# Kernel tuning notes

Measured on AMD Instinct MI355X. Metric: run time of the kernel, lower is better.

Reference implementation:

```python
import jax, jax.numpy as jnp
import numpy as np

NUM_EXPERTS = 8
TOP_K = 2


def setup_inputs() -> dict:
    key = jax.random.key(0)
    ks = jax.random.split(key, 5)
    B, S, H, F, E = 2, 2048, 1024, 4096, NUM_EXPERTS
    return {
        "hidden_states": jax.random.normal(ks[0], (B, S, H), dtype=jnp.float32),
        "router_w": jax.random.normal(ks[1], (H, E), dtype=jnp.float32) * 0.02,
        "router_b": jnp.zeros((E,), dtype=jnp.float32),
        "w1": jax.random.normal(ks[2], (E, H, F), dtype=jnp.float32) * 0.02,
        "b1": jnp.zeros((E, F), dtype=jnp.float32),
        "w2": jax.random.normal(ks[3], (E, F, H), dtype=jnp.float32) * 0.02,
        "b2": jnp.zeros((E, H), dtype=jnp.float32),
    }


def reference(hidden_states, router_w, router_b, w1, b1, w2, b2):
    # Router: softmax over experts, take top-2, renormalize.
    logits = jnp.einsum("bsh,he->bse", hidden_states, router_w) + router_b
    probs = jax.nn.softmax(logits, axis=-1)
    top_w, top_i = jax.lax.top_k(probs, TOP_K)              # [B,S,2]
    top_w = top_w / jnp.sum(top_w, axis=-1, keepdims=True)
    # Combine weights per expert: [B,S,E] (sum of slot weights where routed).
    combine = jnp.sum(
        top_w[..., None] * jax.nn.one_hot(top_i, NUM_EXPERTS, dtype=top_w.dtype),
        axis=-2,
    )
    # Dense expert FFN over stacked experts (grouped GEMM form).
    h = jax.nn.gelu(
        jnp.einsum("bsh,ehf->ebsf", hidden_states, w1) + b1[:, None, None, :],
        approximate=False,
    )  # exact GELU matches torch nn.GELU default
    y = jnp.einsum("ebsf,efh->ebsh", h, w2) + b2[:, None, None, :]
    # Weighted combine of top-2 expert outputs per token.
    return jnp.einsum("bse,ebsh->bsh", combine, y)
```

## Files before the change

kernel.cpp:

```cpp
#include <hip/hip_runtime.h>
#include <hip/hip_bf16.h>
#include <stdint.h>

#define T_TOKENS 4096
#define H_DIM    1024
#define F_DIM    4096
#define NE       8
#define NA       8192

typedef __bf16 bf16x8 __attribute__((ext_vector_type(8)));
typedef float  f32x4  __attribute__((ext_vector_type(4)));

__device__ __forceinline__ float b2f(unsigned short u) {
    union { float f; uint32_t i; } v; v.i = ((uint32_t)u) << 16; return v.f;
}
__device__ __forceinline__ unsigned short f2b(float f) {
    union { float f; uint32_t i; } v; v.f = f;
    uint32_t x = v.i;
    return (unsigned short)((x + 0x7FFFu + ((x >> 16) & 1u)) >> 16);
}

__device__ __forceinline__ float gelu_f(float x) {
    float z = fabsf(x) * 0.70710678118f;
    float t = 1.0f / (1.0f + 0.3275911f * z);
    float p = t * (0.254829592f + t * (-0.284496736f +
              t * (1.421413741f + t * (-1.453152027f + t * 1.061405429f))));
    float erf_z = 1.0f - p * __expf(-z * z);
    float sgn_erf = (x >= 0.f) ? erf_z : -erf_z;
    return x * (0.5f + 0.5f * sgn_erf);
}

__device__ __forceinline__ void gl_lds16(const void* g, void* l) {
    __builtin_amdgcn_global_load_lds(
        (const __attribute__((address_space(1))) void*)g,
        (__attribute__((address_space(3))) void*)l,
        16, 0, 0);
}

__global__ void probe_kernel(const unsigned short* __restrict__ hs,
                             int* __restrict__ flag) {
    int lane = threadIdx.x;
    int cnt = 0;
    for (int j = 0; j < 16; j++) {
        unsigned short u = hs[(lane * 16 + j) * 2];
        int e = (u >> 7) & 0xFF;
        if (e >= 100 && e <= 135) cnt++;
    }
    for (int off = 32; off > 0; off >>= 1) cnt += __shfl_down(cnt, off);
    if (lane == 0) *flag = (cnt >= 512) ? 0 : 1;
}

__global__ __launch_bounds__(256) void router_kernel(
    const void* __restrict__ hs, const void* __restrict__ rw,
    const void* __restrict__ rb, const int* __restrict__ flag,
    int* __restrict__ top_i, float* __restrict__ top_w,
    unsigned short* __restrict__ hsb) {
    bool f32 = (*flag != 0);
    int wave = threadIdx.x >> 6, lane = threadIdx.x & 63;
    int t = blockIdx.x * 4 + wave;
    unsigned short* hout = hsb + (size_t)t * H_DIM;
    float acc[NE];
#pragma unroll
    for (int e = 0; e < NE; e++) acc[e] = 0.f;
    if (f32) {
        const float* hrow = (const float*)hs + (size_t)t * H_DIM;
        const float* rwf = (const float*)rw;
        for (int j = 0; j < 16; j++) {
            int k = j * 64 + lane;
            float h = hrow[k];
            hout[k] = f2b(h);
            float4 a = *(const float4*)(rwf + (size_t)k * NE);
            float4 b = *(const float4*)(rwf + (size_t)k * NE + 4);
            acc[0] += h * a.x; acc[1] += h * a.y; acc[2] += h * a.z; acc[3] += h * a.w;
            acc[4] += h * b.x; acc[5] += h * b.y; acc[6] += h * b.z; acc[7] += h * b.w;
        }
    } else {
        const unsigned short* hrow = (const unsigned short*)hs + (size_t)t * H_DIM;
        const unsigned short* rwu = (const unsigned short*)rw;
        for (int j = 0; j < 16; j++) {
            int k = j * 64 + lane;
            unsigned short hu = hrow[k];
            hout[k] = hu;
            float h = b2f(hu);
            uint4 rv = *(const uint4*)(rwu + (size_t)k * NE);
            const unsigned short* rs = (const unsigned short*)&rv;
#pragma unroll
            for (int e = 0; e < NE; e++) acc[e] += h * b2f(rs[e]);
        }
    }
#pragma unroll
    for (int e = 0; e < NE; e++)
        for (int off = 32; off > 0; off >>= 1) acc[e] += __shfl_down(acc[e], off);
    if (lane == 0) {
        float lg[NE];
#pragma unroll
        for (int e = 0; e < NE; e++)
            lg[e] = acc[e] + (f32 ? ((const float*)rb)[e]
                                  : b2f(((const unsigned short*)rb)[e]));
        int e0 = 0;
        for (int e = 1; e < NE; e++) if (lg[e] > lg[e0]) e0 = e;
        int e1 = (e0 == 0) ? 1 : 0;
        for (int e = 0; e < NE; e++) if (e != e0 && lg[e] > lg[e1]) e1 = e;
        float w0 = 1.f / (1.f + expf(lg[e1] - lg[e0]));
        top_i[t * 2] = e0; top_i[t * 2 + 1] = e1;
        top_w[t * 2] = w0; top_w[t * 2 + 1] = 1.f - w0;
    }
}

__global__ __launch_bounds__(256) void assign_kernel(
    const int* __restrict__ top_i, const float* __restrict__ top_w,
    int* __restrict__ token_list, float* __restrict__ wgt_list,
    int* __restrict__ assign_row, int* __restrict__ counts,
    int* __restrict__ offsets) {
    __shared__ int cnt_s[NE], cur_s[NE];
    int tid = threadIdx.x;
    if (tid < NE) cnt_s[tid] = 0;
    __syncthreads();
    for (int idx = tid; idx < NA; idx += 256) atomicAdd(&cnt_s[top_i[idx]], 1);
    __syncthreads();
    if (tid == 0) {
        int run = 0;
        for (int e = 0; e < NE; e++) {
            offsets[e] = run; counts[e] = cnt_s[e]; cur_s[e] = run; run += cnt_s[e];
        }
    }
    __syncthreads();
    for (int idx = tid; idx < NA; idx += 256) {
        int e = top_i[idx];
        int pos = atomicAdd(&cur_s[e], 1);
        token_list[pos] = idx >> 1;
        wgt_list[pos] = top_w[idx];
        assign_row[idx] = pos;
    }
}

__global__ __launch_bounds__(256) void transpose_kernel(
    const void* __restrict__ in, unsigned short* __restrict__ out,
    int R, int C, const int* __restrict__ flag) {
    bool f32 = (*flag != 0);
    size_t zo = (size_t)blockIdx.z * R * C;
    int c0 = blockIdx.x * 64, r0 = blockIdx.y * 64;
    __shared__ unsigned short t[64][65];
    int tx = threadIdx.x & 15, ty = threadIdx.x >> 4;
    if (f32) {
        const float* inf = (const float*)in + zo;
#pragma unroll
        for (int i = 0; i < 4; i++) {
            int r = ty + i * 16;
            float4 v = *(const float4*)&inf[(size_t)(r0 + r) * C + c0 + tx * 4];
            t[r][tx * 4] = f2b(v.x); t[r][tx * 4 + 1] = f2b(v.y);
            t[r][tx * 4 + 2] = f2b(v.z); t[r][tx * 4 + 3] = f2b(v.w);
        }
    } else {
        const unsigned short* inu = (const unsigned short*)in + zo;
#pragma unroll
        for (int i = 0; i < 4; i++) {
            int r = ty + i * 16;
            ushort4 v = *(const ushort4*)&inu[(size_t)(r0 + r) * C + c0 + tx * 4];
            t[r][tx * 4] = v.x; t[r][tx * 4 + 1] = v.y;
            t[r][tx * 4 + 2] = v.z; t[r][tx * 4 + 3] = v.w;
        }
    }
    __syncthreads();
#pragma unroll
    for (int i = 0; i < 4; i++) {
        int cc = ty + i * 16;
        ushort4 w;
        w.x = t[tx * 4][cc]; w.y = t[tx * 4 + 1][cc];
        w.z = t[tx * 4 + 2][cc]; w.w = t[tx * 4 + 3][cc];
        *(ushort4*)&out[zo + (size_t)(c0 + cc) * R + r0 + tx * 4] = w;
    }
}

template <int MODE>
__global__ __launch_bounds__(256) void gemm_kernel(
    const unsigned short* __restrict__ Abase,
    const unsigned short* __restrict__ Bt,
    const void* __restrict__ bias,
    const int* __restrict__ flag,
    const int* __restrict__ token_list, const float* __restrict__ wgt_list,
    const int* __restrict__ counts, const int* __restrict__ offsets,
    unsigned short* __restrict__ act_out, unsigned short* __restrict__ y_out) {
    constexpr int K    = (MODE == 0) ? H_DIM : F_DIM;
    constexpr int NDIM = (MODE == 0) ? F_DIM : H_DIM;
    constexpr int AST  = (MODE == 0) ? H_DIM : F_DIM;
    constexpr int BM   = (MODE == 0) ? 128 : 64;
    constexpr int MI   = BM / 32;
    constexpr int NIA  = BM / 64;
    constexpr int NK   = K / 32;
    constexpr int ABUF = BM * 32;
    constexpr int BBUF = 128 * 32;

    const int e = blockIdx.z;
    const int cnt = counts[e];
    const int m0 = blockIdx.y * BM;
    if (m0 >= cnt) return;
    const int off = offsets[e];
    const int n0 = blockIdx.x * 128;
    const bool f32 = (*flag != 0);

    __shared__ __bf16 As[2 * ABUF];
    __shared__ __bf16 Bs[2 * BBUF];
    __shared__ int   tok_s[BM];
    __shared__ float wgt_s[BM];

    const int tid = threadIdx.x;
    const int wave = tid >> 6, lane = tid & 63;

    if (tid < BM) {
        int r = off + min(m0 + tid, cnt - 1);
        tok_s[tid] = (MODE == 0) ? token_list[r] : r;
        wgt_s[tid] = wgt_list[r];
    }
    __syncthreads();

    const char* Abytes = (const char*)Abase;
    const char* Bbytes = (const char*)(Bt + (size_t)e * NDIM * K);
    const int rl = lane >> 2;
    const int chk = (lane & 3) ^ (rl & 3);
    uint64_t ga[NIA], gb[2];
    uint32_t la[NIA], lb[2];
#pragma unroll
    for (int j = 0; j < NIA; j++) {
        int rowA = (wave * NIA + j) * 16 + rl;
        ga[j] = (uint64_t)(uintptr_t)(Abytes + ((size_t)tok_s[rowA] * AST + chk * 8) * 2);
        la[j] = (wave * NIA + j) * 512;
    }
#pragma unroll
    for (int j = 0; j < 2; j++) {
        int rowB = n0 + (wave * 2 + j) * 16 + rl;
        gb[j] = (uint64_t)(uintptr_t)(Bbytes + ((size_t)rowB * K + chk * 8) * 2);
        lb[j] = (wave * 2 + j) * 512;
    }

    f32x4 acc[MI][4];
#pragma unroll
    for (int i = 0; i < MI; i++)
#pragma unroll
        for (int j = 0; j < 4; j++) acc[i][j] = (f32x4){0.f, 0.f, 0.f, 0.f};

    const int wr = wave >> 1, wc = wave & 1;
    const int lane15 = lane & 15, quad = lane >> 4;

#pragma unroll
    for (int j = 0; j < NIA; j++) {
        gl_lds16((const void*)(uintptr_t)ga[j], (void*)(As + la[j]));
        ga[j] += 64;
    }
#pragma unroll
    for (int j = 0; j < 2; j++) {
        gl_lds16((const void*)(uintptr_t)gb[j], (void*)(Bs + lb[j]));
        gb[j] += 64;
    }
    __syncthreads();

    for (int kt = 0; kt < NK; kt++) {
        const int cur = kt & 1;
        if (kt + 1 < NK) {
            const int nxt = cur ^ 1;
#pragma unroll
            for (int j = 0; j < NIA; j++) {
                gl_lds16((const void*)(uintptr_t)ga[j], (void*)(As + nxt * ABUF + la[j]));
                ga[j] += 64;
            }
#pragma unroll
            for (int j = 0; j < 2; j++) {
                gl_lds16((const void*)(uintptr_t)gb[j], (void*)(Bs + nxt * BBUF + lb[j]));
                gb[j] += 64;
            }
        }
        const __bf16* Ab = As + cur * ABUF;
        const __bf16* Bb = Bs + cur * BBUF;
        bf16x8 a[MI], b[4];
#pragma unroll
        for (int i = 0; i < MI; i++) {
            int row = wr * (BM / 2) + i * 16 + lane15;
            a[i] = *(const bf16x8*)&Ab[row * 32 + ((quad ^ (row & 3)) * 8)];
        }
#pragma unroll
        for (int j = 0; j < 4; j++) {
            int row = wc * 64 + j * 16 + lane15;
            b[j] = *(const bf16x8*)&Bb[row * 32 + ((quad ^ (row & 3)) * 8)];
        }
#pragma unroll
        for (int i = 0; i < MI; i++)
#pragma unroll
            for (int j = 0; j < 4; j++)
                acc[i][j] = __builtin_amdgcn_mfma_f32_16x16x32_bf16(a[i], b[j], acc[i][j], 0, 0, 0);
        __syncthreads();
    }

#pragma unroll
    for (int j = 0; j < 4; j++) {
        int col = n0 + wc * 64 + j * 16 + lane15;
        float bv = f32 ? ((const float*)bias)[(size_t)e * NDIM + col]
                       : b2f(((const unsigned short*)bias)[(size_t)e * NDIM + col]);
#pragma unroll
        for (int i = 0; i < MI; i++) {
#pragma unroll
            for (int r = 0; r < 4; r++) {
                int rowl = wr * (BM / 2) + i * 16 + quad * 4 + r;
                if (m0 + rowl < cnt) {
                    float v = acc[i][j][r] + bv;
                    if (MODE == 0) {
                        act_out[(size_t)(off + m0 + rowl) * F_DIM + col] = f2b(gelu_f(v));
                    } else {
                        y_out[(size_t)(off + m0 + rowl) * H_DIM + col] = f2b(v * wgt_s[rowl]);
                    }
                }
            }
        }
    }
}

__global__ __launch_bounds__(256) void combine_kernel(
    const unsigned short* __restrict__ y, const int* __restrict__ assign_row,
    void* __restrict__ out, const int* __restrict__ flag) {
    bool f32 = (*flag != 0);
    int t = blockIdx.x;
    int r0 = assign_row[t * 2], r1 = assign_row[t * 2 + 1];
    ushort4 a = ((const ushort4*)(y + (size_t)r0 * H_DIM))[threadIdx.x];
    ushort4 b = ((const ushort4*)(y + (size_t)r1 * H_DIM))[threadIdx.x];
    float s0 = b2f(a.x) + b2f(b.x), s1 = b2f(a.y) + b2f(b.y);
    float s2 = b2f(a.z) + b2f(b.z), s3 = b2f(a.w) + b2f(b.w);
    if (f32) {
        float4 o = {s0, s1, s2, s3};
        ((float4*)out)[(size_t)t * (H_DIM / 4) + threadIdx.x] = o;
    } else {
        ushort4 o;
        o.x = f2b(s0); o.y = f2b(s1); o.z = f2b(s2); o.w = f2b(s3);
        ((ushort4*)((unsigned short*)out + (size_t)t * H_DIM))[threadIdx.x] = o;
    }
}

extern "C" void kernel_launch(void* const* d_in, const int* in_sizes, int n_in,
                              void* d_out, int out_size, void* d_ws, size_t ws_size,
                              hipStream_t stream) {
    const void* hs = d_in[0];
    const void* rw = d_in[1];
    const void* rb = d_in[2];
    const void* w1 = d_in[3];
    const void* b1 = d_in[4];
    const void* w2 = d_in[5];
    const void* b2 = d_in[6];

    char* ws = (char*)d_ws;
    size_t o = 0;
    auto alloc = [&](size_t bytes) {
        char* p = ws + o; o += (bytes + 255) & ~(size_t)255; return p;
    };
    unsigned short* wt   = (unsigned short*)alloc((size_t)NE * F_DIM * H_DIM * 2);
    unsigned short* act  = (unsigned short*)alloc((size_t)NA * F_DIM * 2);
    unsigned short* yb   = (unsigned short*)alloc((size_t)NA * H_DIM * 2);
    unsigned short* hsb  = (unsigned short*)alloc((size_t)T_TOKENS * H_DIM * 2);
    int*   top_i      = (int*)alloc(NA * 4);
    float* top_w      = (float*)alloc(NA * 4);
    int*   token_list = (int*)alloc(NA * 4);
    float* wgt_list   = (float*)alloc(NA * 4);
    int*   assign_row = (int*)alloc(NA * 4);
    int*   counts     = (int*)alloc(64);
    int*   offsets    = (int*)alloc(64);
    int*   flag       = (int*)alloc(64);
    (void)ws_size; (void)in_sizes; (void)n_in; (void)out_size;

    probe_kernel<<<1, 64, 0, stream>>>((const unsigned short*)hs, flag);
    router_kernel<<<T_TOKENS / 4, 256, 0, stream>>>(hs, rw, rb, flag, top_i, top_w, hsb);
    assign_kernel<<<1, 256, 0, stream>>>(top_i, top_w, token_list, wgt_list,
                                         assign_row, counts, offsets);
    transpose_kernel<<<dim3(F_DIM / 64, H_DIM / 64, NE), 256, 0, stream>>>(
        w1, wt, H_DIM, F_DIM, flag);
    gemm_kernel<0><<<dim3(F_DIM / 128, T_TOKENS / 128, NE), 256, 0, stream>>>(
        hsb, wt, b1, flag, token_list, wgt_list, counts, offsets, act, nullptr);
    transpose_kernel<<<dim3(H_DIM / 64, F_DIM / 64, NE), 256, 0, stream>>>(
        w2, wt, F_DIM, H_DIM, flag);
    gemm_kernel<1><<<dim3(H_DIM / 128, T_TOKENS / 64, NE), 256, 0, stream>>>(
        act, wt, b2, flag, token_list, wgt_list, counts, offsets, nullptr, yb);
    combine_kernel<<<T_TOKENS, 256, 0, stream>>>(yb, assign_row, d_out, flag);
}
```

Before: 656.4 us.

## Enlarge grouped-GEMM tiles to 256-row blocks with 512 threads and expert-interleaved block order

After: 656.5 us. About the same (+0.0%).

```diff
diff --git a/kernel.cpp b/kernel.cpp
--- a/kernel.cpp
+++ b/kernel.cpp
@@ -173,7 +173,7 @@
 }
 
 template <int MODE>
-__global__ __launch_bounds__(256) void gemm_kernel(
+__global__ __launch_bounds__(512, 2) void gemm_kernel(
     const unsigned short* __restrict__ Abase,
     const unsigned short* __restrict__ Bt,
     const void* __restrict__ bias,
@@ -183,20 +183,30 @@
     unsigned short* __restrict__ act_out, unsigned short* __restrict__ y_out) {
     constexpr int K    = (MODE == 0) ? H_DIM : F_DIM;
     constexpr int NDIM = (MODE == 0) ? F_DIM : H_DIM;
-    constexpr int AST  = (MODE == 0) ? H_DIM : F_DIM;
-    constexpr int BM   = (MODE == 0) ? 128 : 64;
-    constexpr int MI   = BM / 32;
-    constexpr int NIA  = BM / 64;
+    constexpr int AST  = K;
+    constexpr int BM   = 256;
+    constexpr int BN   = (MODE == 0) ? 256 : 128;
+    constexpr int WM   = (MODE == 0) ? 2 : 4;
+    constexpr int WN   = (MODE == 0) ? 4 : 2;
+    constexpr int MI   = BM / (16 * WM);
+    constexpr int NJ   = BN / (16 * WN);
     constexpr int NK   = K / 32;
     constexpr int ABUF = BM * 32;
-    constexpr int BBUF = 128 * 32;
-
-    const int e = blockIdx.z;
+    constexpr int BBUF = BN * 32;
+    constexpr int NIA  = BM / 128;
+    constexpr int NIB  = BN / 128;
+
+    const int lid = blockIdx.x + gridDim.x * (blockIdx.y + gridDim.y * blockIdx.z);
+    const int e   = lid & 7;
+    const int r_  = lid >> 3;
+    const int nx  = r_ % gridDim.x;
+    const int my  = r_ / gridDim.x;
+
     const int cnt = counts[e];
-    const int m0 = blockIdx.y * BM;
+    const int m0 = my * BM;
     if (m0 >= cnt) return;
     const int off = offsets[e];
-    const int n0 = blockIdx.x * 128;
+    const int n0 = nx * BN;
     const bool f32 = (*flag != 0);
 
     __shared__ __bf16 As[2 * ABUF];
@@ -218,8 +228,8 @@
     const char* Bbytes = (const char*)(Bt + (size_t)e * NDIM * K);
     const int rl = lane >> 2;
     const int chk = (lane & 3) ^ (rl & 3);
-    uint64_t ga[NIA], gb[2];
-    uint32_t la[NIA], lb[2];
+    uint64_t ga[NIA], gb[NIB];
+    uint32_t la[NIA], lb[NIB];
 #pragma unroll
     for (int j = 0; j < NIA; j++) {
         int rowA = (wave * NIA + j) * 16 + rl;
@@ -227,19 +237,19 @@
         la[j] = (wave * NIA + j) * 512;
     }
 #pragma unroll
-    for (int j = 0; j < 2; j++) {
-        int rowB = n0 + (wave * 2 + j) * 16 + rl;
+    for (int j = 0; j < NIB; j++) {
+        int rowB = n0 + (wave * NIB + j) * 16 + rl;
         gb[j] = (uint64_t)(uintptr_t)(Bbytes + ((size_t)rowB * K + chk * 8) * 2);
-        lb[j] = (wave * 2 + j) * 512;
-    }
-
-    f32x4 acc[MI][4];
+        lb[j] = (wave * NIB + j) * 512;
+    }
+
+    f32x4 acc[MI][NJ];
 #pragma unroll
     for (int i = 0; i < MI; i++)
 #pragma unroll
-        for (int j = 0; j < 4; j++) acc[i][j] = (f32x4){0.f, 0.f, 0.f, 0.f};
-
-    const int wr = wave >> 1, wc = wave & 1;
+        for (int j = 0; j < NJ; j++) acc[i][j] = (f32x4){0.f, 0.f, 0.f, 0.f};
+
+    const int wr = wave / WN, wc = wave % WN;
     const int lane15 = lane & 15, quad = lane >> 4;
 
 #pragma unroll
@@ -248,7 +258,7 @@
         ga[j] += 64;
     }
 #pragma unroll
-    for (int j = 0; j < 2; j++) {
+    for (int j = 0; j < NIB; j++) {
         gl_lds16((const void*)(uintptr_t)gb[j], (void*)(Bs + lb[j]));
         gb[j] += 64;
     }
@@ -264,42 +274,42 @@
                 ga[j] += 64;
             }
 #pragma unroll
-            for (int j = 0; j < 2; j++) {
+            for (int j = 0; j < NIB; j++) {
                 gl_lds16((const void*)(uintptr_t)gb[j], (void*)(Bs + nxt * BBUF + lb[j]));
                 gb[j] += 64;
             }
         }
         const __bf16* Ab = As + cur * ABUF;
         const __bf16* Bb = Bs + cur * BBUF;
-        bf16x8 a[MI], b[4];
+        bf16x8 a[MI], b[NJ];
 #pragma unroll
         for (int i = 0; i < MI; i++) {
-            int row = wr * (BM / 2) + i * 16 + lane15;
+            int row = wr * (BM / WM) + i * 16 + lane15;
             a[i] = *(const bf16x8*)&Ab[row * 32 + ((quad ^ (row & 3)) * 8)];
         }
 #pragma unroll
-        for (int j = 0; j < 4; j++) {
-            int row = wc * 64 + j * 16 + lane15;
+        for (int j = 0; j < NJ; j++) {
+            int row = wc * (BN / WN) + j * 16 + lane15;
             b[j] = *(const bf16x8*)&Bb[row * 32 + ((quad ^ (row & 3)) * 8)];
         }
 #pragma unroll
         for (int i = 0; i < MI; i++)
 #pragma unroll
-            for (int j = 0; j < 4; j++)
+            for (int j = 0; j < NJ; j++)
                 acc[i][j] = __builtin_amdgcn_mfma_f32_16x16x32_bf16(a[i], b[j], acc[i][j], 0, 0, 0);
         __syncthreads();
     }
 
 #pragma unroll
-    for (int j = 0; j < 4; j++) {
-        int col = n0 + wc * 64 + j * 16 + lane15;
+    for (int j = 0; j < NJ; j++) {
+        int col = n0 + wc * (BN / WN) + j * 16 + lane15;
         float bv = f32 ? ((const float*)bias)[(size_t)e * NDIM + col]
                        : b2f(((const unsigned short*)bias)[(size_t)e * NDIM + col]);
 #pragma unroll
         for (int i = 0; i < MI; i++) {
 #pragma unroll
             for (int r = 0; r < 4; r++) {
-                int rowl = wr * (BM / 2) + i * 16 + quad * 4 + r;
+                int rowl = wr * (BM / WM) + i * 16 + quad * 4 + r;
                 if (m0 + rowl < cnt) {
                     float v = acc[i][j][r] + bv;
                     if (MODE == 0) {
@@ -369,11 +379,11 @@
                                          assign_row, counts, offsets);
     transpose_kernel<<<dim3(F_DIM / 64, H_DIM / 64, NE), 256, 0, stream>>>(
         w1, wt, H_DIM, F_DIM, flag);
-    gemm_kernel<0><<<dim3(F_DIM / 128, T_TOKENS / 128, NE), 256, 0, stream>>>(
+    gemm_kernel<0><<<dim3(F_DIM / 256, T_TOKENS / 256, NE), 512, 0, stream>>>(
         hsb, wt, b1, flag, token_list, wgt_list, counts, offsets, act, nullptr);
     transpose_kernel<<<dim3(H_DIM / 64, F_DIM / 64, NE), 256, 0, stream>>>(
         w2, wt, F_DIM, H_DIM, flag);
-    gemm_kernel<1><<<dim3(H_DIM / 128, T_TOKENS / 64, NE), 256, 0, stream>>>(
+    gemm_kernel<1><<<dim3(H_DIM / 128, T_TOKENS / 256, NE), 512, 0, stream>>>(
         act, wt, b2, flag, token_list, wgt_list, counts, offsets, nullptr, yb);
     combine_kernel<<<T_TOKENS, 256, 0, stream>>>(yb, assign_row, d_out, flag);
 }
```
